# Performance work log

Hardware: AMD Instinct MI355X
Metric: run time of the kernel (lower is better)

The kernel has to match this reference:

```python
import jax, jax.numpy as jnp
import numpy as np

B, L, D = 1, 4096, 1024
N_AR, N_DIFF, D_HEAD = 8, 8, 64
H = N_AR + N_DIFF
ROPE_BASE = 10000.0


def rotate_half(x):
    x1, x2 = jnp.split(x, 2, axis=-1)
    return jnp.concatenate([-x2, x1], axis=-1)


def rope_cos_sin(seq_len, d_head):
    inv_freq = 1.0 / (ROPE_BASE ** (jnp.arange(0, d_head, 2, dtype=jnp.float32) / d_head))
    t = jnp.arange(seq_len, dtype=jnp.float32)
    freqs = t[:, None] * inv_freq[None, :]          # [L, d_head//2]
    emb = jnp.concatenate([freqs, freqs], axis=-1)  # [L, d_head]
    return jnp.cos(emb), jnp.sin(emb)


def setup_inputs() -> dict:
    key = jax.random.key(0)
    ks = jax.random.split(key, 5)
    return {
        "hidden_states": jax.random.normal(ks[0], (B, L, D), dtype=jnp.float32),
        "Wq": jax.random.normal(ks[1], (D, H * D_HEAD), dtype=jnp.float32) * 0.02,
        "Wk": jax.random.normal(ks[2], (D, H * D_HEAD), dtype=jnp.float32) * 0.02,
        "Wv": jax.random.normal(ks[3], (D, H * D_HEAD), dtype=jnp.float32) * 0.02,
        "Wo": jax.random.normal(ks[4], (H * D_HEAD, D), dtype=jnp.float32) * 0.02,
    }


def _attend(q, k, v, mask):
    # q,k,v: [B, h, L, d]; mask: [L, L] additive
    scale = D_HEAD ** -0.5
    scores = jnp.einsum("bhqd,bhkd->bhqk", q, k) * scale + mask
    attn = jax.nn.softmax(scores.astype(jnp.float32), axis=-1).astype(q.dtype)
    return jnp.einsum("bhqk,bhkd->bhqd", attn, v)


def reference(hidden_states, Wq, Wk, Wv, Wo):
    b, l, _ = hidden_states.shape

    def heads(x, W):
        return (x @ W).reshape(b, l, H, D_HEAD).transpose(0, 2, 1, 3)  # [B,H,L,d]

    q = heads(hidden_states, Wq)
    k = heads(hidden_states, Wk)
    v = heads(hidden_states, Wv)

    cos, sin = rope_cos_sin(l, D_HEAD)  # [L, d]
    q = q * cos + rotate_half(q) * sin
    k = k * cos + rotate_half(k) * sin

    neg_inf = jnp.finfo(jnp.float32).min
    causal = jnp.where(jnp.tril(jnp.ones((l, l), dtype=bool)), 0.0, -jnp.inf).astype(jnp.float32)

    out_ar = _attend(q[:, :N_AR], k[:, :N_AR], v[:, :N_AR], causal)
    out_diff = _attend(q[:, N_AR:], k[:, N_AR:], v[:, N_AR:], jnp.zeros((l, l), jnp.float32))

    out = jnp.concatenate([out_ar, out_diff], axis=1)          # [B,H,L,d]
    out = out.transpose(0, 2, 1, 3).reshape(b, l, H * D_HEAD)  # [B,L,H*d]
    return out @ Wo
```

## Files before the change

kernel.cpp:

```cpp
#include <hip/hip_runtime.h>

#define LSEQ 4096
#define DMODEL 1024
#define HTOT 16
#define NAR 8
#define DHEAD 64
#define QKVS 3072

typedef unsigned short u16;
typedef unsigned int u32;
typedef __attribute__((ext_vector_type(8))) short bf16x8;
typedef __attribute__((ext_vector_type(4))) float f32x4;

typedef __attribute__((address_space(1))) void gvoid;
typedef __attribute__((address_space(3))) void lvoid;

__device__ __forceinline__ void cp16(const void* g, void* l) {
    __builtin_amdgcn_global_load_lds((gvoid*)(void*)g, (lvoid*)l, 16, 0, 0);
}

__device__ __forceinline__ float bfs(u16 v) { return __uint_as_float((u32)v << 16); }
__device__ __forceinline__ u16 f2bf(float f) {
    u32 x = __float_as_uint(f);
    return (u16)((x + 0x7fffu + ((x >> 16) & 1u)) >> 16);
}
__device__ __forceinline__ u32 pack2(float a, float b) {
    return (u32)f2bf(a) | ((u32)f2bf(b) << 16);
}

__global__ __launch_bounds__(256) void transp_cvt(
    const float* __restrict__ S, u16* __restrict__ D)
{
    __shared__ u16 T[64][72];
    const int tid = threadIdx.x;
    const int bx = blockIdx.x, by = blockIdx.y;
#pragma unroll
    for (int i = 0; i < 4; ++i) {
        int id = tid + i * 256;
        int fr = id >> 4, fc = id & 15;
        float4 v = *(const float4*)(S + (size_t)(by * 64 + fr) * 1024 + bx * 64 + fc * 4);
        T[fc * 4 + 0][fr] = f2bf(v.x);
        T[fc * 4 + 1][fr] = f2bf(v.y);
        T[fc * 4 + 2][fr] = f2bf(v.z);
        T[fc * 4 + 3][fr] = f2bf(v.w);
    }
    __syncthreads();
#pragma unroll
    for (int i = 0; i < 2; ++i) {
        int id = tid + i * 256;
        int c = id >> 3, g = id & 7;
        *(uint4*)(D + (size_t)(bx * 64 + c) * 1024 + by * 64 + g * 8) = *(const uint4*)&T[c][g * 8];
    }
}

__global__ __launch_bounds__(256) void gemm_qkv(
    const float* __restrict__ A, const u16* __restrict__ Bt, u16* __restrict__ C)
{
    __shared__ u16 As[128][40];
    __shared__ u16 Bs[128][32];
    const int tid = threadIdx.x;
    const int lane = tid & 63, w = tid >> 6;
    const int col = lane & 15, quad = lane >> 4;
    const int bm = blockIdx.y << 7, bn = blockIdx.x << 7;
    const int wm = (w & 1) << 6, wn = (w >> 1) << 6;
    const int sr = lane >> 2, sc = (lane & 3) << 3;
    const f32x4 zero = {0.f, 0.f, 0.f, 0.f};
    f32x4 acc[4][4];
#pragma unroll
    for (int i = 0; i < 4; ++i)
#pragma unroll
        for (int j = 0; j < 4; ++j) acc[i][j] = zero;

    const int ar0 = tid >> 2, ag = (tid & 3) << 3;

    for (int k0 = 0; k0 < 1024; k0 += 32) {
        float4 a0[2], a1[2];
#pragma unroll
        for (int it = 0; it < 2; ++it) {
            const float* ap = A + (size_t)(bm + ar0 + it * 64) * 1024 + k0 + ag;
            a0[it] = *(const float4*)ap;
            a1[it] = *(const float4*)(ap + 4);
        }
        __syncthreads();
#pragma unroll
        for (int i = 0; i < 2; ++i) {
            int r0 = w * 32 + i * 16;
            cp16(Bt + (size_t)(bn + r0 + sr) * 1024 + k0 + sc, &Bs[r0][0]);
        }
#pragma unroll
        for (int it = 0; it < 2; ++it) {
            uint4 pk;
            pk.x = pack2(a0[it].x, a0[it].y); pk.y = pack2(a0[it].z, a0[it].w);
            pk.z = pack2(a1[it].x, a1[it].y); pk.w = pack2(a1[it].z, a1[it].w);
            *(uint4*)&As[ar0 + it * 64][ag] = pk;
        }
        __syncthreads();
        bf16x8 af[4], bfr[4];
#pragma unroll
        for (int i = 0; i < 4; ++i) af[i] = *(const bf16x8*)&As[wm + i * 16 + col][quad * 8];
#pragma unroll
        for (int j = 0; j < 4; ++j) bfr[j] = *(const bf16x8*)&Bs[wn + j * 16 + col][quad * 8];
#pragma unroll
        for (int i = 0; i < 4; ++i)
#pragma unroll
            for (int j = 0; j < 4; ++j)
                acc[i][j] = __builtin_amdgcn_mfma_f32_16x16x32_bf16(af[i], bfr[j], acc[i][j], 0, 0, 0);
    }
#pragma unroll
    for (int i = 0; i < 4; ++i)
#pragma unroll
        for (int j = 0; j < 4; ++j)
#pragma unroll
            for (int r = 0; r < 4; ++r)
                C[(size_t)(bm + wm + i * 16 + quad * 4 + r) * QKVS + bn + wn + j * 16 + col] =
                    f2bf(acc[i][j][r]);
}

__global__ __launch_bounds__(256) void gemm_out(
    const u16* __restrict__ A, const u16* __restrict__ Bt, float* __restrict__ C)
{
    __shared__ u16 As[128][32];
    __shared__ u16 Bs[128][32];
    const int tid = threadIdx.x;
    const int lane = tid & 63, w = tid >> 6;
    const int col = lane & 15, quad = lane >> 4;
    const int bm = blockIdx.y << 7, bn = blockIdx.x << 7;
    const int wm = (w & 1) << 6, wn = (w >> 1) << 6;
    const int sr = lane >> 2, sc = (lane & 3) << 3;
    const f32x4 zero = {0.f, 0.f, 0.f, 0.f};
    f32x4 acc[4][4];
#pragma unroll
    for (int i = 0; i < 4; ++i)
#pragma unroll
        for (int j = 0; j < 4; ++j) acc[i][j] = zero;

    for (int k0 = 0; k0 < 1024; k0 += 32) {
        __syncthreads();
#pragma unroll
        for (int i = 0; i < 2; ++i) {
            int r0 = w * 32 + i * 16;
            cp16(A  + (size_t)(bm + r0 + sr) * 1024 + k0 + sc, &As[r0][0]);
            cp16(Bt + (size_t)(bn + r0 + sr) * 1024 + k0 + sc, &Bs[r0][0]);
        }
        __syncthreads();
        bf16x8 af[4], bfr[4];
#pragma unroll
        for (int i = 0; i < 4; ++i) af[i] = *(const bf16x8*)&As[wm + i * 16 + col][quad * 8];
#pragma unroll
        for (int j = 0; j < 4; ++j) bfr[j] = *(const bf16x8*)&Bs[wn + j * 16 + col][quad * 8];
#pragma unroll
        for (int i = 0; i < 4; ++i)
#pragma unroll
            for (int j = 0; j < 4; ++j)
                acc[i][j] = __builtin_amdgcn_mfma_f32_16x16x32_bf16(af[i], bfr[j], acc[i][j], 0, 0, 0);
    }
#pragma unroll
    for (int i = 0; i < 4; ++i)
#pragma unroll
        for (int j = 0; j < 4; ++j)
#pragma unroll
            for (int r = 0; r < 4; ++r)
                C[(size_t)(bm + wm + i * 16 + quad * 4 + r) * 1024 + bn + wn + j * 16 + col] =
                    acc[i][j][r];
}

__global__ __launch_bounds__(256) void rope_kernel(u16* __restrict__ QKV)
{
    const int idx = blockIdx.x * 256 + threadIdx.x;
    const int i = idx & 31;
    const int h = (idx >> 5) & 15;
    const int t = idx >> 9;
    const float inv = __expf((float)i * -0.2878231366242557f);
    float s, c;
    __sincosf((float)t * inv, &s, &c);
    const size_t base = (size_t)t * QKVS + h * DHEAD + i;

    float q1 = bfs(QKV[base]), q2 = bfs(QKV[base + 32]);
    QKV[base]      = f2bf((q1 * c - q2 * s) * 0.125f);
    QKV[base + 32] = f2bf((q2 * c + q1 * s) * 0.125f);

    const size_t kb = base + 1024;
    float k1 = bfs(QKV[kb]), k2 = bfs(QKV[kb + 32]);
    QKV[kb]      = f2bf(k1 * c - k2 * s);
    QKV[kb + 32] = f2bf(k2 * c + k1 * s);
}

__global__ __launch_bounds__(256) void attn_mfma(
    const u16* __restrict__ QKV, u16* __restrict__ AO)
{
    __shared__ u16 Ks[64][72];
    __shared__ u16 Vt[80][72];
    __shared__ u16 Ps[4][32][72];
    const int qt = blockIdx.x, h = blockIdx.y;
    const bool causal = (h < NAR);
    const int tid = threadIdx.x;
    const int w = tid >> 6, lane = tid & 63;
    const int col = lane & 15, quad = lane >> 4;
    const int qbase = qt * 128 + w * 32;

    {
        int row = 64 + (tid >> 4);
        u32 val = (row == 64) ? 0x3F803F80u : 0u;
        u32* p = (u32*)&Vt[row][(tid & 15) * 4];
        p[0] = val; p[1] = val;
    }

    bf16x8 qf[2][2];
#pragma unroll
    for (int im = 0; im < 2; ++im)
#pragma unroll
        for (int ks = 0; ks < 2; ++ks)
            qf[im][ks] = *(const bf16x8*)(QKV + (size_t)(qbase + im * 16 + col) * QKVS +
                                          h * DHEAD + ks * 32 + quad * 8);

    const f32x4 zero = {0.f, 0.f, 0.f, 0.f};
    f32x4 O[2][5];
#pragma unroll
    for (int im = 0; im < 2; ++im)
#pragma unroll
        for (int nd = 0; nd < 5; ++nd) O[im][nd] = zero;

    const int nch = causal ? (qt * 2 + 2) : (LSEQ / 64);
    const int kv_kp = tid & 31, kv_dg = tid >> 5;
    u16* pb = &Ps[w][quad * 4][col];

    for (int ch = 0; ch < nch; ++ch) {
        __syncthreads();
#pragma unroll
        for (int it = 0; it < 2; ++it) {
            int id = tid + it * 256;
            int r = id >> 3, g = id & 7;
            *(uint4*)&Ks[r][g * 8] =
                *(const uint4*)(QKV + (size_t)(ch * 64 + r) * QKVS + 1024 + h * DHEAD + g * 8);
        }
        {
            const u16* vp = QKV + (size_t)(ch * 64 + kv_kp * 2) * QKVS + 2048 + h * DHEAD + kv_dg * 8;
            bf16x8 v0 = *(const bf16x8*)vp;
            bf16x8 v1 = *(const bf16x8*)(vp + QKVS);
#pragma unroll
            for (int j = 0; j < 8; ++j)
                *(u32*)&Vt[kv_dg * 8 + j][kv_kp * 2] =
                    (u32)(u16)v0[j] | ((u32)(u16)v1[j] << 16);
        }
        __syncthreads();

        f32x4 s[2][4];
#pragma unroll
        for (int im = 0; im < 2; ++im)
#pragma unroll
            for (int jn = 0; jn < 4; ++jn) s[im][jn] = zero;
#pragma unroll
        for (int jn = 0; jn < 4; ++jn)
#pragma unroll
            for (int ks = 0; ks < 2; ++ks) {
                bf16x8 kf = *(const bf16x8*)&Ks[jn * 16 + col][ks * 32 + quad * 8];
                s[0][jn] = __builtin_amdgcn_mfma_f32_16x16x32_bf16(qf[0][ks], kf, s[0][jn], 0, 0, 0);
                s[1][jn] = __builtin_amdgcn_mfma_f32_16x16x32_bf16(qf[1][ks], kf, s[1][jn], 0, 0, 0);
            }
        if (causal && ch * 64 + 63 > qbase) {
#pragma unroll
            for (int im = 0; im < 2; ++im)
#pragma unroll
                for (int jn = 0; jn < 4; ++jn) {
                    int kk = ch * 64 + jn * 16 + col;
#pragma unroll
                    for (int r = 0; r < 4; ++r) {
                        int qq = qbase + im * 16 + quad * 4 + r;
                        if (kk > qq) s[im][jn][r] = -1e30f;
                    }
                }
        }
#pragma unroll
        for (int im = 0; im < 2; ++im)
#pragma unroll
            for (int jn = 0; jn < 4; ++jn)
#pragma unroll
                for (int r = 0; r < 4; ++r)
                    pb[(im * 16 + r) * 72 + jn * 16] = f2bf(__expf(s[im][jn][r]));
#pragma unroll
        for (int ks = 0; ks < 2; ++ks) {
            bf16x8 pa0 = *(const bf16x8*)&Ps[w][col][ks * 32 + quad * 8];
            bf16x8 pa1 = *(const bf16x8*)&Ps[w][16 + col][ks * 32 + quad * 8];
#pragma unroll
            for (int nd = 0; nd < 5; ++nd) {
                bf16x8 vf = *(const bf16x8*)&Vt[nd * 16 + col][ks * 32 + quad * 8];
                O[0][nd] = __builtin_amdgcn_mfma_f32_16x16x32_bf16(pa0, vf, O[0][nd], 0, 0, 0);
                O[1][nd] = __builtin_amdgcn_mfma_f32_16x16x32_bf16(pa1, vf, O[1][nd], 0, 0, 0);
            }
        }
    }
#pragma unroll
    for (int im = 0; im < 2; ++im)
#pragma unroll
        for (int r = 0; r < 4; ++r) {
            float l = __shfl(O[im][4][r], 0, 16);
            float inv = 1.f / l;
            int row = im * 16 + quad * 4 + r;
#pragma unroll
            for (int nd = 0; nd < 4; ++nd)
                Ps[w][row][nd * 16 + col] = f2bf(O[im][nd][r] * inv);
        }
#pragma unroll
    for (int i = 0; i < 4; ++i) {
        int id = lane + i * 64;
        int row = id >> 3, g = id & 7;
        *(uint4*)(AO + (size_t)(qt * 128 + w * 32 + row) * 1024 + h * DHEAD + g * 8) =
            *(const uint4*)&Ps[w][row][g * 8];
    }
}

extern "C" void kernel_launch(void* const* d_in, const int* in_sizes, int n_in,
                              void* d_out, int out_size, void* d_ws, size_t ws_size,
                              hipStream_t stream)
{
    const float* X  = (const float*)d_in[0];
    const float* Wq = (const float*)d_in[1];
    const float* Wk = (const float*)d_in[2];
    const float* Wv = (const float*)d_in[3];
    const float* Wo = (const float*)d_in[4];
    float* out = (float*)d_out;

    u16* Wt  = (u16*)d_ws;
    u16* AOb = (u16*)d_ws;
    u16* QKV = (u16*)d_ws + (size_t)4 * 1024 * 1024;
    u16* Wot = QKV;

    dim3 t16(16, 16);
    transp_cvt<<<t16, 256, 0, stream>>>(Wq, Wt);
    transp_cvt<<<t16, 256, 0, stream>>>(Wk, Wt + 1024 * 1024);
    transp_cvt<<<t16, 256, 0, stream>>>(Wv, Wt + 2 * 1024 * 1024);
    gemm_qkv<<<dim3(24, 32), 256, 0, stream>>>(X, Wt, QKV);
    rope_kernel<<<(LSEQ * HTOT * 32) / 256, 256, 0, stream>>>(QKV);
    attn_mfma<<<dim3(32, 16), 256, 0, stream>>>(QKV, AOb);
    transp_cvt<<<t16, 256, 0, stream>>>(Wo, Wot);
    gemm_out<<<dim3(8, 32), 256, 0, stream>>>(AOb, Wot, out);
}
```

Before: 300.9 us.

## Double-buffer GEMM and attention loads, swizzle K smem, use exp2, rebalance attention blocks

Both GEMMs and the attention loop now prefetch the next K-chunk into a second shared-memory buffer while computing the current one, removing one barrier per iteration. Attention loads K asynchronously with an XOR-swizzled layout to reduce LDS bank conflicts. It folds log2(e) into the Q scale so it can use the native exp2. Attention blocks are reordered so the heaviest causal tiles are scheduled among the non-causal ones. The three weight transposes are merged into one launch. Double buffering raises shared-memory use, which may reduce occupancy.

```diff
diff --git a/kernel.cpp b/kernel.cpp
--- a/kernel.cpp
+++ b/kernel.cpp
@@ -28,10 +28,13 @@
     return (u32)f2bf(a) | ((u32)f2bf(b) << 16);
 }
 
-__global__ __launch_bounds__(256) void transp_cvt(
-    const float* __restrict__ S, u16* __restrict__ D)
+__global__ __launch_bounds__(256) void transp_cvt3(
+    const float* __restrict__ Wq, const float* __restrict__ Wk,
+    const float* __restrict__ Wv, u16* __restrict__ D)
 {
     __shared__ u16 T[64][72];
+    const float* S = (blockIdx.z == 0) ? Wq : ((blockIdx.z == 1) ? Wk : Wv);
+    u16* Dz = D + (size_t)blockIdx.z * 1024 * 1024;
     const int tid = threadIdx.x;
     const int bx = blockIdx.x, by = blockIdx.y;
 #pragma unroll
@@ -49,6 +52,31 @@
     for (int i = 0; i < 2; ++i) {
         int id = tid + i * 256;
         int c = id >> 3, g = id & 7;
+        *(uint4*)(Dz + (size_t)(bx * 64 + c) * 1024 + by * 64 + g * 8) = *(const uint4*)&T[c][g * 8];
+    }
+}
+
+__global__ __launch_bounds__(256) void transp_cvt(
+    const float* __restrict__ S, u16* __restrict__ D)
+{
+    __shared__ u16 T[64][72];
+    const int tid = threadIdx.x;
+    const int bx = blockIdx.x, by = blockIdx.y;
+#pragma unroll
+    for (int i = 0; i < 4; ++i) {
+        int id = tid + i * 256;
+        int fr = id >> 4, fc = id & 15;
+        float4 v = *(const float4*)(S + (size_t)(by * 64 + fr) * 1024 + bx * 64 + fc * 4);
+        T[fc * 4 + 0][fr] = f2bf(v.x);
+        T[fc * 4 + 1][fr] = f2bf(v.y);
+        T[fc * 4 + 2][fr] = f2bf(v.z);
+        T[fc * 4 + 3][fr] = f2bf(v.w);
+    }
+    __syncthreads();
+#pragma unroll
+    for (int i = 0; i < 2; ++i) {
+        int id = tid + i * 256;
+        int c = id >> 3, g = id & 7;
         *(uint4*)(D + (size_t)(bx * 64 + c) * 1024 + by * 64 + g * 8) = *(const uint4*)&T[c][g * 8];
     }
 }
@@ -56,8 +84,95 @@
 __global__ __launch_bounds__(256) void gemm_qkv(
     const float* __restrict__ A, const u16* __restrict__ Bt, u16* __restrict__ C)
 {
-    __shared__ u16 As[128][40];
-    __shared__ u16 Bs[128][32];
+    __shared__ u16 As[2][128][40];
+    __shared__ u16 Bs[2][128][32];
+    const int tid = threadIdx.x;
+    const int lane = tid & 63, w = tid >> 6;
+    const int col = lane & 15, quad = lane >> 4;
+    const int bm = blockIdx.y << 7, bn = blockIdx.x << 7;
+    const int wm = (w & 1) << 6, wn = (w >> 1) << 6;
+    const int sr = lane >> 2, sc = (lane & 3) << 3;
+    const int ar0 = tid >> 2, ag = (tid & 3) << 3;
+    const f32x4 zero = {0.f, 0.f, 0.f, 0.f};
+    f32x4 acc[4][4];
+#pragma unroll
+    for (int i = 0; i < 4; ++i)
+#pragma unroll
+        for (int j = 0; j < 4; ++j) acc[i][j] = zero;
+
+    {
+#pragma unroll
+        for (int i = 0; i < 2; ++i)
+            cp16(Bt + (size_t)(bn + w * 32 + i * 16 + sr) * 1024 + sc, &Bs[0][w * 32 + i * 16][0]);
+        float4 a0[2], a1[2];
+#pragma unroll
+        for (int it = 0; it < 2; ++it) {
+            const float* ap = A + (size_t)(bm + ar0 + it * 64) * 1024 + ag;
+            a0[it] = *(const float4*)ap;
+            a1[it] = *(const float4*)(ap + 4);
+        }
+#pragma unroll
+        for (int it = 0; it < 2; ++it) {
+            uint4 pk;
+            pk.x = pack2(a0[it].x, a0[it].y); pk.y = pack2(a0[it].z, a0[it].w);
+            pk.z = pack2(a1[it].x, a1[it].y); pk.w = pack2(a1[it].z, a1[it].w);
+            *(uint4*)&As[0][ar0 + it * 64][ag] = pk;
+        }
+    }
+
+    for (int kc = 0; kc < 32; ++kc) {
+        const int cur = kc & 1, nxt = cur ^ 1;
+        __syncthreads();
+        const bool pre = (kc + 1 < 32);
+        float4 a0[2], a1[2];
+        if (pre) {
+            const int k1 = (kc + 1) * 32;
+#pragma unroll
+            for (int i = 0; i < 2; ++i)
+                cp16(Bt + (size_t)(bn + w * 32 + i * 16 + sr) * 1024 + k1 + sc,
+                     &Bs[nxt][w * 32 + i * 16][0]);
+#pragma unroll
+            for (int it = 0; it < 2; ++it) {
+                const float* ap = A + (size_t)(bm + ar0 + it * 64) * 1024 + k1 + ag;
+                a0[it] = *(const float4*)ap;
+                a1[it] = *(const float4*)(ap + 4);
+            }
+        }
+        bf16x8 af[4], bfr[4];
+#pragma unroll
+        for (int i = 0; i < 4; ++i) af[i] = *(const bf16x8*)&As[cur][wm + i * 16 + col][quad * 8];
+#pragma unroll
+        for (int j = 0; j < 4; ++j) bfr[j] = *(const bf16x8*)&Bs[cur][wn + j * 16 + col][quad * 8];
+#pragma unroll
+        for (int i = 0; i < 4; ++i)
+#pragma unroll
+            for (int j = 0; j < 4; ++j)
+                acc[i][j] = __builtin_amdgcn_mfma_f32_16x16x32_bf16(af[i], bfr[j], acc[i][j], 0, 0, 0);
+        if (pre) {
+#pragma unroll
+            for (int it = 0; it < 2; ++it) {
+                uint4 pk;
+                pk.x = pack2(a0[it].x, a0[it].y); pk.y = pack2(a0[it].z, a0[it].w);
+                pk.z = pack2(a1[it].x, a1[it].y); pk.w = pack2(a1[it].z, a1[it].w);
+                *(uint4*)&As[nxt][ar0 + it * 64][ag] = pk;
+            }
+        }
+    }
+#pragma unroll
+    for (int i = 0; i < 4; ++i)
+#pragma unroll
+        for (int j = 0; j < 4; ++j)
+#pragma unroll
+            for (int r = 0; r < 4; ++r)
+                C[(size_t)(bm + wm + i * 16 + quad * 4 + r) * QKVS + bn + wn + j * 16 + col] =
+                    f2bf(acc[i][j][r]);
+}
+
+__global__ __launch_bounds__(256) void gemm_out(
+    const u16* __restrict__ A, const u16* __restrict__ Bt, float* __restrict__ C)
+{
+    __shared__ u16 As[2][128][32];
+    __shared__ u16 Bs[2][128][32];
     const int tid = threadIdx.x;
     const int lane = tid & 63, w = tid >> 6;
     const int col = lane & 15, quad = lane >> 4;
@@ -71,83 +186,30 @@
 #pragma unroll
         for (int j = 0; j < 4; ++j) acc[i][j] = zero;
 
-    const int ar0 = tid >> 2, ag = (tid & 3) << 3;
-
-    for (int k0 = 0; k0 < 1024; k0 += 32) {
-        float4 a0[2], a1[2];
-#pragma unroll
-        for (int it = 0; it < 2; ++it) {
-            const float* ap = A + (size_t)(bm + ar0 + it * 64) * 1024 + k0 + ag;
-            a0[it] = *(const float4*)ap;
-            a1[it] = *(const float4*)(ap + 4);
-        }
+#pragma unroll
+    for (int i = 0; i < 2; ++i) {
+        const int r0 = w * 32 + i * 16;
+        cp16(A  + (size_t)(bm + r0 + sr) * 1024 + sc, &As[0][r0][0]);
+        cp16(Bt + (size_t)(bn + r0 + sr) * 1024 + sc, &Bs[0][r0][0]);
+    }
+
+    for (int kc = 0; kc < 32; ++kc) {
+        const int cur = kc & 1, nxt = cur ^ 1;
         __syncthreads();
-#pragma unroll
-        for (int i = 0; i < 2; ++i) {
-            int r0 = w * 32 + i * 16;
-            cp16(Bt + (size_t)(bn + r0 + sr) * 1024 + k0 + sc, &Bs[r0][0]);
-        }
-#pragma unroll
-        for (int it = 0; it < 2; ++it) {
-            uint4 pk;
-            pk.x = pack2(a0[it].x, a0[it].y); pk.y = pack2(a0[it].z, a0[it].w);
-            pk.z = pack2(a1[it].x, a1[it].y); pk.w = pack2(a1[it].z, a1[it].w);
-            *(uint4*)&As[ar0 + it * 64][ag] = pk;
-        }
-        __syncthreads();
+        if (kc + 1 < 32) {
+            const int k1 = (kc + 1) * 32;
+#pragma unroll
+            for (int i = 0; i < 2; ++i) {
+                const int r0 = w * 32 + i * 16;
+                cp16(A  + (size_t)(bm + r0 + sr) * 1024 + k1 + sc, &As[nxt][r0][0]);
+                cp16(Bt + (size_t)(bn + r0 + sr) * 1024 + k1 + sc, &Bs[nxt][r0][0]);
+            }
+        }
         bf16x8 af[4], bfr[4];
 #pragma unroll
-        for (int i = 0; i < 4; ++i) af[i] = *(const bf16x8*)&As[wm + i * 16 + col][quad * 8];
-#pragma unroll
-        for (int j = 0; j < 4; ++j) bfr[j] = *(const bf16x8*)&Bs[wn + j * 16 + col][quad * 8];
-#pragma unroll
-        for (int i = 0; i < 4; ++i)
-#pragma unroll
-            for (int j = 0; j < 4; ++j)
-                acc[i][j] = __builtin_amdgcn_mfma_f32_16x16x32_bf16(af[i], bfr[j], acc[i][j], 0, 0, 0);
-    }
-#pragma unroll
-    for (int i = 0; i < 4; ++i)
-#pragma unroll
-        for (int j = 0; j < 4; ++j)
-#pragma unroll
-            for (int r = 0; r < 4; ++r)
-                C[(size_t)(bm + wm + i * 16 + quad * 4 + r) * QKVS + bn + wn + j * 16 + col] =
-                    f2bf(acc[i][j][r]);
-}
-
-__global__ __launch_bounds__(256) void gemm_out(
-    const u16* __restrict__ A, const u16* __restrict__ Bt, float* __restrict__ C)
-{
-    __shared__ u16 As[128][32];
-    __shared__ u16 Bs[128][32];
-    const int tid = threadIdx.x;
-    const int lane = tid & 63, w = tid >> 6;
-    const int col = lane & 15, quad = lane >> 4;
-    const int bm = blockIdx.y << 7, bn = blockIdx.x << 7;
-    const int wm = (w & 1) << 6, wn = (w >> 1) << 6;
-    const int sr = lane >> 2, sc = (lane & 3) << 3;
-    const f32x4 zero = {0.f, 0.f, 0.f, 0.f};
-    f32x4 acc[4][4];
-#pragma unroll
-    for (int i = 0; i < 4; ++i)
-#pragma unroll
-        for (int j = 0; j < 4; ++j) acc[i][j] = zero;
-
-    for (int k0 = 0; k0 < 1024; k0 += 32) {
-        __syncthreads();
-#pragma unroll
-        for (int i = 0; i < 2; ++i) {
-            int r0 = w * 32 + i * 16;
-            cp16(A  + (size_t)(bm + r0 + sr) * 1024 + k0 + sc, &As[r0][0]);
-            cp16(Bt + (size_t)(bn + r0 + sr) * 1024 + k0 + sc, &Bs[r0][0]);
-        }
-        __syncthreads();
-        bf16x8 af[4], bfr[4];
-#pragma unroll
-        for (int i = 0; i < 4; ++i) af[i] = *(const bf16x8*)&As[wm + i * 16 + col][quad * 8];
-#pragma unroll
-        for (int j = 0; j < 4; ++j) bfr[j] = *(const bf16x8*)&Bs[wn + j * 16 + col][quad * 8];
+        for (int i = 0; i < 4; ++i) af[i] = *(const bf16x8*)&As[cur][wm + i * 16 + col][quad * 8];
+#pragma unroll
+        for (int j = 0; j < 4; ++j) bfr[j] = *(const bf16x8*)&Bs[cur][wn + j * 16 + col][quad * 8];
 #pragma unroll
         for (int i = 0; i < 4; ++i)
 #pragma unroll
@@ -174,10 +236,11 @@
     float s, c;
     __sincosf((float)t * inv, &s, &c);
     const size_t base = (size_t)t * QKVS + h * DHEAD + i;
+    const float qs = 0.18033688011112042f;
 
     float q1 = bfs(QKV[base]), q2 = bfs(QKV[base + 32]);
-    QKV[base]      = f2bf((q1 * c - q2 * s) * 0.125f);
-    QKV[base + 32] = f2bf((q2 * c + q1 * s) * 0.125f);
+    QKV[base]      = f2bf((q1 * c - q2 * s) * qs);
+    QKV[base + 32] = f2bf((q2 * c + q1 * s) * qs);
 
     const size_t kb = base + 1024;
     float k1 = bfs(QKV[kb]), k2 = bfs(QKV[kb + 32]);
@@ -188,10 +251,13 @@
 __global__ __launch_bounds__(256) void attn_mfma(
     const u16* __restrict__ QKV, u16* __restrict__ AO)
 {
-    __shared__ u16 Ks[64][72];
-    __shared__ u16 Vt[80][72];
+    __shared__ u16 Ks[2][64][64];
+    __shared__ u16 Vt[2][80][72];
     __shared__ u16 Ps[4][32][72];
-    const int qt = blockIdx.x, h = blockIdx.y;
+    const int bid = blockIdx.x;
+    int h, qt;
+    if (bid < 256) { h = 8 + (bid & 7); qt = bid >> 3; }
+    else { int i = bid - 256; h = i & 7; qt = 31 - (i >> 3); }
     const bool causal = (h < NAR);
     const int tid = threadIdx.x;
     const int w = tid >> 6, lane = tid & 63;
@@ -201,8 +267,9 @@
     {
         int row = 64 + (tid >> 4);
         u32 val = (row == 64) ? 0x3F803F80u : 0u;
-        u32* p = (u32*)&Vt[row][(tid & 15) * 4];
-        p[0] = val; p[1] = val;
+        u32* p0 = (u32*)&Vt[0][row][(tid & 15) * 4];
+        u32* p1 = (u32*)&Vt[1][row][(tid & 15) * 4];
+        p0[0] = val; p0[1] = val; p1[0] = val; p1[1] = val;
     }
 
     bf16x8 qf[2][2];
@@ -223,26 +290,36 @@
     const int nch = causal ? (qt * 2 + 2) : (LSEQ / 64);
     const int kv_kp = tid & 31, kv_dg = tid >> 5;
     u16* pb = &Ps[w][quad * 4][col];
+    const int krow = lane >> 3;
+    const int kcb = (lane & 7) ^ krow;
+    const u16* kbase = QKV + (size_t)krow * QKVS + 1024 + h * DHEAD + kcb * 8;
+
+    {
+#pragma unroll
+        for (int i = 0; i < 2; ++i)
+            cp16(kbase + (size_t)((i * 4 + w) * 8) * QKVS, &Ks[0][(i * 4 + w) * 8][0]);
+        const u16* vp = QKV + (size_t)(kv_kp * 2) * QKVS + 2048 + h * DHEAD + kv_dg * 8;
+        bf16x8 v0 = *(const bf16x8*)vp;
+        bf16x8 v1 = *(const bf16x8*)(vp + QKVS);
+#pragma unroll
+        for (int j = 0; j < 8; ++j)
+            *(u32*)&Vt[0][kv_dg * 8 + j][kv_kp * 2] = (u32)(u16)v0[j] | ((u32)(u16)v1[j] << 16);
+    }
 
     for (int ch = 0; ch < nch; ++ch) {
+        const int cur = ch & 1, nxt = cur ^ 1;
         __syncthreads();
-#pragma unroll
-        for (int it = 0; it < 2; ++it) {
-            int id = tid + it * 256;
-            int r = id >> 3, g = id & 7;
-            *(uint4*)&Ks[r][g * 8] =
-                *(const uint4*)(QKV + (size_t)(ch * 64 + r) * QKVS + 1024 + h * DHEAD + g * 8);
-        }
-        {
-            const u16* vp = QKV + (size_t)(ch * 64 + kv_kp * 2) * QKVS + 2048 + h * DHEAD + kv_dg * 8;
-            bf16x8 v0 = *(const bf16x8*)vp;
-            bf16x8 v1 = *(const bf16x8*)(vp + QKVS);
-#pragma unroll
-            for (int j = 0; j < 8; ++j)
-                *(u32*)&Vt[kv_dg * 8 + j][kv_kp * 2] =
-                    (u32)(u16)v0[j] | ((u32)(u16)v1[j] << 16);
-        }
-        __syncthreads();
+        const bool pre = (ch + 1 < nch);
+        bf16x8 v0 = {}, v1 = {};
+        if (pre) {
+            const int c1 = (ch + 1) * 64;
+#pragma unroll
+            for (int i = 0; i < 2; ++i)
+                cp16(kbase + (size_t)(c1 + (i * 4 + w) * 8) * QKVS, &Ks[nxt][(i * 4 + w) * 8][0]);
+            const u16* vp = QKV + (size_t)(c1 + kv_kp * 2) * QKVS + 2048 + h * DHEAD + kv_dg * 8;
+            v0 = *(const bf16x8*)vp;
+            v1 = *(const bf16x8*)(vp + QKVS);
+        }
 
         f32x4 s[2][4];
 #pragma unroll
@@ -253,7 +330,7 @@
         for (int jn = 0; jn < 4; ++jn)
 #pragma unroll
             for (int ks = 0; ks < 2; ++ks) {
-                bf16x8 kf = *(const bf16x8*)&Ks[jn * 16 + col][ks * 32 + quad * 8];
+                bf16x8 kf = *(const bf16x8*)&Ks[cur][jn * 16 + col][((ks * 4 + quad) ^ (col & 7)) * 8];
                 s[0][jn] = __builtin_amdgcn_mfma_f32_16x16x32_bf16(qf[0][ks], kf, s[0][jn], 0, 0, 0);
                 s[1][jn] = __builtin_amdgcn_mfma_f32_16x16x32_bf16(qf[1][ks], kf, s[1][jn], 0, 0, 0);
             }
@@ -276,17 +353,24 @@
             for (int jn = 0; jn < 4; ++jn)
 #pragma unroll
                 for (int r = 0; r < 4; ++r)
-                    pb[(im * 16 + r) * 72 + jn * 16] = f2bf(__expf(s[im][jn][r]));
+                    pb[(im * 16 + r) * 72 + jn * 16] =
+                        f2bf(__builtin_amdgcn_exp2f(s[im][jn][r]));
 #pragma unroll
         for (int ks = 0; ks < 2; ++ks) {
             bf16x8 pa0 = *(const bf16x8*)&Ps[w][col][ks * 32 + quad * 8];
             bf16x8 pa1 = *(const bf16x8*)&Ps[w][16 + col][ks * 32 + quad * 8];
 #pragma unroll
             for (int nd = 0; nd < 5; ++nd) {
-                bf16x8 vf = *(const bf16x8*)&Vt[nd * 16 + col][ks * 32 + quad * 8];
+                bf16x8 vf = *(const bf16x8*)&Vt[cur][nd * 16 + col][ks * 32 + quad * 8];
                 O[0][nd] = __builtin_amdgcn_mfma_f32_16x16x32_bf16(pa0, vf, O[0][nd], 0, 0, 0);
                 O[1][nd] = __builtin_amdgcn_mfma_f32_16x16x32_bf16(pa1, vf, O[1][nd], 0, 0, 0);
             }
+        }
+        if (pre) {
+#pragma unroll
+            for (int j = 0; j < 8; ++j)
+                *(u32*)&Vt[nxt][kv_dg * 8 + j][kv_kp * 2] =
+                    (u32)(u16)v0[j] | ((u32)(u16)v1[j] << 16);
         }
     }
 #pragma unroll
@@ -325,13 +409,10 @@
     u16* QKV = (u16*)d_ws + (size_t)4 * 1024 * 1024;
     u16* Wot = QKV;
 
-    dim3 t16(16, 16);
-    transp_cvt<<<t16, 256, 0, stream>>>(Wq, Wt);
-    transp_cvt<<<t16, 256, 0, stream>>>(Wk, Wt + 1024 * 1024);
-    transp_cvt<<<t16, 256, 0, stream>>>(Wv, Wt + 2 * 1024 * 1024);
+    transp_cvt3<<<dim3(16, 16, 3), 256, 0, stream>>>(Wq, Wk, Wv, Wt);
     gemm_qkv<<<dim3(24, 32), 256, 0, stream>>>(X, Wt, QKV);
     rope_kernel<<<(LSEQ * HTOT * 32) / 256, 256, 0, stream>>>(QKV);
-    attn_mfma<<<dim3(32, 16), 256, 0, stream>>>(QKV, AOb);
-    transp_cvt<<<t16, 256, 0, stream>>>(Wo, Wot);
+    attn_mfma<<<512, 256, 0, stream>>>(QKV, AOb);
+    transp_cvt<<<dim3(16, 16), 256, 0, stream>>>(Wo, Wot);
     gemm_out<<<dim3(8, 32), 256, 0, stream>>>(AOb, Wot, out);
 }
```

Measured after the change: 292.9 us. 1.03x faster.
